# Performance work log

Measured on AMD Instinct MI355X. Metric: run time of the kernel, lower is better.

## Reference

```python
import jax, jax.numpy as jnp
import numpy as np

IN_DIM = 512
HID = IN_DIM // 2
N_SCENES = 64
SEG_LEN = 4096
N = N_SCENES * SEG_LEN
EPS = 1e-5


def setup_inputs() -> dict:
    key = jax.random.key(0)
    ks = jax.random.split(key, 6)
    feats = jax.random.normal(ks[0], (N, IN_DIM), dtype=jnp.float32)
    offsets = (jnp.arange(N_SCENES + 1, dtype=jnp.int32) * SEG_LEN)
    ln_g = jnp.ones((IN_DIM,), jnp.float32) + 0.02 * jax.random.normal(ks[1], (IN_DIM,), jnp.float32)
    ln_b = 0.02 * jax.random.normal(ks[2], (IN_DIM,), jnp.float32)
    w1 = jax.random.normal(ks[3], (HID, IN_DIM), jnp.float32) / np.sqrt(IN_DIM)
    b1 = jnp.zeros((HID,), jnp.float32)
    w2 = jax.random.normal(ks[4], (1, HID), jnp.float32) / np.sqrt(HID)
    b2 = jnp.zeros((1,), jnp.float32)
    return {"feats": feats, "ln_g": ln_g, "ln_b": ln_b, "w1": w1, "b1": b1, "w2": w2, "b2": b2, "offsets": offsets}


def reference(feats, ln_g, ln_b, w1, b1, w2, b2, offsets):
    n = feats.shape[0]
    # segment id per point from prefix-sum offsets
    seg = jnp.searchsorted(offsets, jnp.arange(n, dtype=offsets.dtype), side="right") - 1
    # score MLP: LayerNorm -> Linear -> GELU(exact) -> Linear -> scalar
    mu = jnp.mean(feats, axis=-1, keepdims=True)
    var = jnp.mean(jnp.square(feats - mu), axis=-1, keepdims=True)
    x = (feats - mu) * jax.lax.rsqrt(var + EPS) * ln_g + ln_b
    h = jax.nn.gelu(x @ w1.T + b1, approximate=False)  # [N, HID]
    s = (h @ w2.T + b2)[:, 0]  # [N]
    # segment softmax (stable)
    smax = jax.ops.segment_max(s, seg, num_segments=N_SCENES)
    e = jnp.exp(s - smax[seg])
    denom = jax.ops.segment_sum(e, seg, num_segments=N_SCENES)
    w = e / denom[seg]
    # weighted sum per segment -> [N_SCENES, IN_DIM]
    pooled = jax.ops.segment_sum(feats * w[:, None], seg, num_segments=N_SCENES)
    return pooled
```

## Files before the change

### kernel.cpp

```cpp
#include <hip/hip_runtime.h>

#define IN_DIM 512
#define HID_DIM 256
#define ROWS 32
#define XSS 520

typedef __bf16 bf16x8 __attribute__((ext_vector_type(8)));
typedef unsigned short ushort8 __attribute__((ext_vector_type(8)));
typedef float floatx16 __attribute__((ext_vector_type(16)));

__device__ __forceinline__ unsigned short f2bf_rne(float x) {
    unsigned int u = __float_as_uint(x);
    u += 0x7FFFu + ((u >> 16) & 1u);
    return (unsigned short)(u >> 16);
}
__device__ __forceinline__ unsigned int pack_bf2(float lo, float hi) {
    const unsigned int u0 = __float_as_uint(lo) + 0x8000u;
    const unsigned int u1 = __float_as_uint(hi) + 0x8000u;
    return __builtin_amdgcn_perm(u1, u0, 0x07060302u);
}
__device__ __forceinline__ float gelu(float x) {
    const float ax = fabsf(x) * 0.70710678118654752f;
    const float t = __builtin_amdgcn_rcpf(1.0f + 0.3275911f * ax);
    const float y = t * (0.254829592f +
                    t * (-0.284496736f +
                    t * (1.421413741f +
                    t * (-1.453152027f + t * 1.061405429f))));
    const float e = __expf(-ax * ax);
    float er = 1.0f - y * e;
    er = __builtin_copysignf(er, x);
    return 0.5f * x * (1.0f + er);
}

__global__ void prep_w1_kernel(const float* __restrict__ w1, const float* __restrict__ ln_g,
                               const float* __restrict__ ln_b, const float* __restrict__ b1,
                               unsigned short* __restrict__ w1g, float* __restrict__ gw,
                               float* __restrict__ c1) {
    const int wid = threadIdx.x >> 6;
    const int lane = threadIdx.x & 63;
    const int h = blockIdx.x * 4 + wid;
    const int c8 = lane * 8;
    const float4 wv0 = *(const float4*)(w1 + (size_t)h * IN_DIM + c8);
    const float4 wv1 = *(const float4*)(w1 + (size_t)h * IN_DIM + c8 + 4);
    const float4 g0 = *(const float4*)(ln_g + c8);
    const float4 g1 = *(const float4*)(ln_g + c8 + 4);
    const float4 bb0 = *(const float4*)(ln_b + c8);
    const float4 bb1 = *(const float4*)(ln_b + c8 + 4);
    float wg[8] = {wv0.x * g0.x, wv0.y * g0.y, wv0.z * g0.z, wv0.w * g0.w,
                   wv1.x * g1.x, wv1.y * g1.y, wv1.z * g1.z, wv1.w * g1.w};
    float sg = wg[0] + wg[1] + wg[2] + wg[3] + wg[4] + wg[5] + wg[6] + wg[7];
    float sb = wv0.x * bb0.x + wv0.y * bb0.y + wv0.z * bb0.z + wv0.w * bb0.w +
               wv1.x * bb1.x + wv1.y * bb1.y + wv1.z * bb1.z + wv1.w * bb1.w;
    ushort8 outv;
#pragma unroll
    for (int j = 0; j < 8; j++) outv[j] = f2bf_rne(wg[j]);
    *(ushort8*)(w1g + (size_t)h * IN_DIM + c8) = outv;
    for (int m = 32; m; m >>= 1) {
        sg += __shfl_xor(sg, m);
        sb += __shfl_xor(sb, m);
    }
    if (lane == 0) {
        gw[h] = sg;
        c1[h] = sb + b1[h];
    }
}

__global__ __launch_bounds__(512, 2) void score_kernel(
    const float* __restrict__ feats, const unsigned short* __restrict__ w1g,
    const float* __restrict__ gw, const float* __restrict__ c1,
    const float* __restrict__ w2, const float* __restrict__ b2,
    float* __restrict__ s_out, int N, int ntiles) {
    __shared__ unsigned short xs[ROWS][XSS];
    __shared__ float2 stats_s[ROWS];
    __shared__ float spart[8][ROWS];

    const int tid = threadIdx.x;
    const int wid = tid >> 6;
    const int lane = tid & 63;
    const int l31 = lane & 31;
    const int hi = lane >> 5;
    const int hid = wid * 32 + l31;

    const float gwv = gw[hid];
    const float c1v = c1[hid];
    const float w2v = w2[hid];
    const float b2v = b2[0];

    bf16x8 barr[32];
    {
        const unsigned short* bp = w1g + (size_t)hid * IN_DIM + hi * 8;
#pragma unroll
        for (int ki = 0; ki < 32; ki++)
            barr[ki] = __builtin_bit_cast(bf16x8, *(const ushort8*)(bp + ki * 16));
    }

    const int srow = tid >> 4;
    const int schunk = tid & 15;

    for (int t = blockIdx.x; t < ntiles; t += gridDim.x) {
        const int row0 = t * ROWS;

        {
            size_t rg = (size_t)(row0 + srow);
            if (rg >= (size_t)N) rg = (size_t)N - 1;
            const float* fp = feats + rg * IN_DIM + schunk * 4;
            float4 f[8];
#pragma unroll
            for (int j = 0; j < 8; j++) f[j] = *(const float4*)(fp + j * 64);
            float sf = 0.0f, qf = 0.0f;
#pragma unroll
            for (int j = 0; j < 8; j++) {
                sf += f[j].x + f[j].y + f[j].z + f[j].w;
                qf = fmaf(f[j].x, f[j].x, qf);
                qf = fmaf(f[j].y, f[j].y, qf);
                qf = fmaf(f[j].z, f[j].z, qf);
                qf = fmaf(f[j].w, f[j].w, qf);
            }
#pragma unroll
            for (int j = 0; j < 8; j++) {
                uint2 p;
                p.x = pack_bf2(f[j].x, f[j].y);
                p.y = pack_bf2(f[j].z, f[j].w);
                *(uint2*)&xs[srow][j * 64 + schunk * 4] = p;
            }
#pragma unroll
            for (int m = 1; m < 16; m <<= 1) {
                sf += __shfl_xor(sf, m);
                qf += __shfl_xor(qf, m);
            }
            if (schunk == 0) {
                const float mu = sf * (1.0f / IN_DIM);
                const float var = fmaxf(qf * (1.0f / IN_DIM) - mu * mu, 0.0f);
                stats_s[srow] = make_float2(mu, rsqrtf(var + 1e-5f));
            }
        }
        __syncthreads();

        floatx16 acc = (floatx16)(0.0f);
        {
            const unsigned short* ap = &xs[l31][hi * 8];
#pragma unroll
            for (int ki = 0; ki < 32; ki++) {
                const bf16x8 af = __builtin_bit_cast(bf16x8, *(const ushort8*)(ap + ki * 16));
                acc = __builtin_amdgcn_mfma_f32_32x32x16_bf16(af, barr[ki], acc, 0, 0, 0);
            }
        }

        float tv[16];
#pragma unroll
        for (int r = 0; r < 16; r++) {
            const int row = (r & 3) + 8 * (r >> 2) + 4 * hi;
            const float2 st = stats_s[row];
            const float hv = st.y * (acc[r] - st.x * gwv) + c1v;
            tv[r] = gelu(hv) * w2v;
        }
#pragma unroll
        for (int m = 1; m < 32; m <<= 1)
#pragma unroll
            for (int r = 0; r < 16; r++) tv[r] += __shfl_xor(tv[r], m);
        if (l31 == 0) {
#pragma unroll
            for (int r = 0; r < 16; r++)
                spart[wid][(r & 3) + 8 * (r >> 2) + 4 * hi] = tv[r];
        }
        __syncthreads();
        if (tid < ROWS) {
            const int row = row0 + tid;
            if (row < N) {
                float sv = b2v;
#pragma unroll
                for (int w = 0; w < 8; w++) sv += spart[w][tid];
                s_out[row] = sv;
            }
        }
    }
}

__global__ void segstat_kernel(const float* __restrict__ s, const int* __restrict__ offsets,
                               float* __restrict__ smax, float* __restrict__ denom, int nseg) {
    const int seg = blockIdx.x;
    const int st = offsets[seg];
    const int en = offsets[seg + 1];
    const int tid = threadIdx.x;
    __shared__ float red[8];
    float m = -3.4e38f;
    for (int i = st + tid; i < en; i += 256) m = fmaxf(m, s[i]);
    for (int mm = 32; mm; mm >>= 1) m = fmaxf(m, __shfl_xor(m, mm));
    if ((tid & 63) == 0) red[tid >> 6] = m;
    __syncthreads();
    const float M = fmaxf(fmaxf(red[0], red[1]), fmaxf(red[2], red[3]));
    float sum = 0.0f;
    for (int i = st + tid; i < en; i += 256) sum += expf(s[i] - M);
    for (int mm = 32; mm; mm >>= 1) sum += __shfl_xor(sum, mm);
    if ((tid & 63) == 0) red[4 + (tid >> 6)] = sum;
    __syncthreads();
    if (tid == 0) {
        smax[seg] = M;
        denom[seg] = red[4] + red[5] + red[6] + red[7];
    }
}

#define CHUNK 256
__global__ __launch_bounds__(256) void pool_kernel(
    const float* __restrict__ feats, const float* __restrict__ s,
    const float* __restrict__ smax, const float* __restrict__ denom,
    const int* __restrict__ offsets, int nseg, float* __restrict__ out, int N) {
    __shared__ float wbuf[CHUNK];
    __shared__ int sbuf[CHUNK];
    const int tid = threadIdx.x;
    const int r0 = blockIdx.x * CHUNK;
    const int nrows = min(CHUNK, N - r0);

    {
        const int row = r0 + tid;
        float wv = 0.0f;
        int sg = 0;
        if (row < N) {
            int lo = 0, hiq = nseg;
            while (hiq - lo > 1) {
                const int mid = (lo + hiq) >> 1;
                if (offsets[mid] <= row) lo = mid; else hiq = mid;
            }
            sg = lo;
            wv = expf(s[row] - smax[sg]) / denom[sg];
        }
        wbuf[tid] = wv;
        sbuf[tid] = sg;
    }
    __syncthreads();

    const int c4 = (tid & 127) * 4;
    const int half = tid >> 7;
    const int rs = half * (CHUNK / 2);
    const int re = min(rs + CHUNK / 2, nrows);
    if (re <= rs) return;

    if (sbuf[0] == sbuf[nrows - 1]) {
        const int seg = sbuf[0];
        float ax = 0.0f, ay = 0.0f, az = 0.0f, aw = 0.0f;
        const float* fp = feats + (size_t)r0 * IN_DIM + c4;
#pragma unroll 4
        for (int r = rs; r < re; r++) {
            const float4 f = *(const float4*)(fp + (size_t)r * IN_DIM);
            const float wv = wbuf[r];
            ax = fmaf(wv, f.x, ax);
            ay = fmaf(wv, f.y, ay);
            az = fmaf(wv, f.z, az);
            aw = fmaf(wv, f.w, aw);
        }
        float* op = out + (size_t)seg * IN_DIM + c4;
        atomicAdd(op + 0, ax);
        atomicAdd(op + 1, ay);
        atomicAdd(op + 2, az);
        atomicAdd(op + 3, aw);
    } else {
        for (int r = rs; r < re; r++) {
            const float4 f = *(const float4*)(feats + (size_t)(r0 + r) * IN_DIM + c4);
            const float wv = wbuf[r];
            float* op = out + (size_t)sbuf[r] * IN_DIM + c4;
            atomicAdd(op + 0, wv * f.x);
            atomicAdd(op + 1, wv * f.y);
            atomicAdd(op + 2, wv * f.z);
            atomicAdd(op + 3, wv * f.w);
        }
    }
}

extern "C" void kernel_launch(void* const* d_in, const int* in_sizes, int n_in,
                              void* d_out, int out_size, void* d_ws, size_t ws_size,
                              hipStream_t stream) {
    const float* feats = (const float*)d_in[0];
    const float* ln_g = (const float*)d_in[1];
    const float* ln_b = (const float*)d_in[2];
    const float* w1 = (const float*)d_in[3];
    const float* b1 = (const float*)d_in[4];
    const float* w2 = (const float*)d_in[5];
    const float* b2 = (const float*)d_in[6];
    const int* offsets = (const int*)d_in[7];
    const int N = in_sizes[0] / IN_DIM;
    const int nseg = in_sizes[7] - 1;
    float* out = (float*)d_out;

    char* ws = (char*)d_ws;
    unsigned short* w1g = (unsigned short*)ws;
    float* gw = (float*)(ws + (size_t)HID_DIM * IN_DIM * 2);
    float* c1 = gw + HID_DIM;
    float* s_arr = c1 + HID_DIM;
    float* smax = s_arr + N;
    float* denom = smax + nseg;

    const int ntiles = (N + ROWS - 1) / ROWS;
    int sgrid = ntiles < 2048 ? ntiles : 2048;

    hipMemsetAsync(d_out, 0, (size_t)out_size * sizeof(float), stream);
    prep_w1_kernel<<<HID_DIM / 4, 256, 0, stream>>>(w1, ln_g, ln_b, b1, w1g, gw, c1);
    score_kernel<<<sgrid, 512, 0, stream>>>(feats, w1g, gw, c1, w2, b2, s_arr, N, ntiles);
    segstat_kernel<<<nseg, 256, 0, stream>>>(s_arr, offsets, smax, denom, nseg);
    pool_kernel<<<(N + CHUNK - 1) / CHUNK, 256, 0, stream>>>(feats, s_arr, smax, denom, offsets, nseg, out, N);
}
```

Measured before the change: 901.9 us.

## Fuse scoring, online segment softmax and pooling into one split-segment kernel

Replaces the score, segstat and pool kernels with a single fused kernel. Each block owns a slice of one segment, computes the scores, keeps a running max and denominator (online softmax), and pools the bf16 copy of feats already staged in LDS. A small combine kernel then merges the per-slice partials. This removes the second full read of feats and the intermediate score array, and drops the atomics and the memset. In exchange, pooling now uses bf16-rounded feats, so precision drops. W1 is streamed from global/L2 on every tile instead of held in registers, and the grid is fixed at 1024 blocks of 256 threads, which may limit occupancy and MFMA throughput.

```diff
diff --git a/kernel.cpp b/kernel.cpp
--- a/kernel.cpp
+++ b/kernel.cpp
@@ -4,6 +4,8 @@
 #define HID_DIM 256
 #define ROWS 32
 #define XSS 520
+#define PSEG 16
+#define PSTRIDE 516
 
 typedef __bf16 bf16x8 __attribute__((ext_vector_type(8)));
 typedef unsigned short ushort8 __attribute__((ext_vector_type(8)));
@@ -65,43 +67,52 @@
     }
 }
 
-__global__ __launch_bounds__(512, 2) void score_kernel(
+__global__ __launch_bounds__(256, 4) void fused_kernel(
     const float* __restrict__ feats, const unsigned short* __restrict__ w1g,
     const float* __restrict__ gw, const float* __restrict__ c1,
     const float* __restrict__ w2, const float* __restrict__ b2,
-    float* __restrict__ s_out, int N, int ntiles) {
+    const int* __restrict__ offsets, float* __restrict__ partials, int N) {
     __shared__ unsigned short xs[ROWS][XSS];
+    __shared__ float spart[4][ROWS];
     __shared__ float2 stats_s[ROWS];
-    __shared__ float spart[8][ROWS];
+    __shared__ float wbuf[ROWS];
+    __shared__ float sMx, sDn, sAl;
 
     const int tid = threadIdx.x;
     const int wid = tid >> 6;
     const int lane = tid & 63;
     const int l31 = lane & 31;
     const int hi = lane >> 5;
-    const int hid = wid * 32 + l31;
-
-    const float gwv = gw[hid];
-    const float c1v = c1[hid];
-    const float w2v = w2[hid];
+    const int seg = blockIdx.x / PSEG;
+    const int part = blockIdx.x % PSEG;
+    const int st = offsets[seg];
+    const int en = offsets[seg + 1];
+    const int len = en - st;
+    const int chunk = (len + PSEG - 1) / PSEG;
+    const int rs = st + part * chunk;
+    const int re = min(rs + chunk, en);
+    const int nt = (re > rs) ? ((re - rs + ROWS - 1) / ROWS) : 0;
+
+    const int hid0 = (wid * 2 + 0) * 32 + l31;
+    const int hid1 = (wid * 2 + 1) * 32 + l31;
+    const float gw0 = gw[hid0], gw1 = gw[hid1];
+    const float c10 = c1[hid0], c11 = c1[hid1];
+    const float w20 = w2[hid0], w21 = w2[hid1];
     const float b2v = b2[0];
 
-    bf16x8 barr[32];
-    {
-        const unsigned short* bp = w1g + (size_t)hid * IN_DIM + hi * 8;
-#pragma unroll
-        for (int ki = 0; ki < 32; ki++)
-            barr[ki] = __builtin_bit_cast(bf16x8, *(const ushort8*)(bp + ki * 16));
-    }
-
-    const int srow = tid >> 4;
+    float O0 = 0.0f, O1 = 0.0f;
+    if (tid == 0) { sMx = -3.0e38f; sDn = 0.0f; }
+
+    const int srow4 = tid >> 4;
     const int schunk = tid & 15;
 
-    for (int t = blockIdx.x; t < ntiles; t += gridDim.x) {
-        const int row0 = t * ROWS;
-
-        {
-            size_t rg = (size_t)(row0 + srow);
+    for (int t = 0; t < nt; t++) {
+        const int row0 = rs + t * ROWS;
+
+#pragma unroll
+        for (int p = 0; p < 2; p++) {
+            const int r = p * 16 + srow4;
+            size_t rg = (size_t)(row0 + r);
             if (rg >= (size_t)N) rg = (size_t)N - 1;
             const float* fp = feats + rg * IN_DIM + schunk * 4;
             float4 f[8];
@@ -118,10 +129,10 @@
             }
 #pragma unroll
             for (int j = 0; j < 8; j++) {
-                uint2 p;
-                p.x = pack_bf2(f[j].x, f[j].y);
-                p.y = pack_bf2(f[j].z, f[j].w);
-                *(uint2*)&xs[srow][j * 64 + schunk * 4] = p;
+                uint2 pk;
+                pk.x = pack_bf2(f[j].x, f[j].y);
+                pk.y = pack_bf2(f[j].z, f[j].w);
+                *(uint2*)&xs[r][j * 64 + schunk * 4] = pk;
             }
 #pragma unroll
             for (int m = 1; m < 16; m <<= 1) {
@@ -131,18 +142,31 @@
             if (schunk == 0) {
                 const float mu = sf * (1.0f / IN_DIM);
                 const float var = fmaxf(qf * (1.0f / IN_DIM) - mu * mu, 0.0f);
-                stats_s[srow] = make_float2(mu, rsqrtf(var + 1e-5f));
-            }
-        }
-        __syncthreads();
-
-        floatx16 acc = (floatx16)(0.0f);
+                stats_s[r] = make_float2(mu, rsqrtf(var + 1e-5f));
+            }
+        }
+        __syncthreads();
+
+        floatx16 acc0 = (floatx16)(0.0f);
+        floatx16 acc1 = (floatx16)(0.0f);
         {
+            const unsigned short* bp0 = w1g + (size_t)hid0 * IN_DIM + hi * 8;
+            const unsigned short* bp1 = w1g + (size_t)hid1 * IN_DIM + hi * 8;
             const unsigned short* ap = &xs[l31][hi * 8];
-#pragma unroll
+            bf16x8 b0 = __builtin_bit_cast(bf16x8, *(const ushort8*)bp0);
+            bf16x8 b1 = __builtin_bit_cast(bf16x8, *(const ushort8*)bp1);
+#pragma unroll 4
             for (int ki = 0; ki < 32; ki++) {
-                const bf16x8 af = __builtin_bit_cast(bf16x8, *(const ushort8*)(ap + ki * 16));
-                acc = __builtin_amdgcn_mfma_f32_32x32x16_bf16(af, barr[ki], acc, 0, 0, 0);
+                const bf16x8 a = __builtin_bit_cast(bf16x8, *(const ushort8*)(ap + ki * 16));
+                bf16x8 n0 = b0, n1 = b1;
+                if (ki < 31) {
+                    n0 = __builtin_bit_cast(bf16x8, *(const ushort8*)(bp0 + (ki + 1) * 16));
+                    n1 = __builtin_bit_cast(bf16x8, *(const ushort8*)(bp1 + (ki + 1) * 16));
+                }
+                acc0 = __builtin_amdgcn_mfma_f32_32x32x16_bf16(a, b0, acc0, 0, 0, 0);
+                acc1 = __builtin_amdgcn_mfma_f32_32x32x16_bf16(a, b1, acc1, 0, 0, 0);
+                b0 = n0;
+                b1 = n1;
             }
         }
 
@@ -150,9 +174,10 @@
 #pragma unroll
         for (int r = 0; r < 16; r++) {
             const int row = (r & 3) + 8 * (r >> 2) + 4 * hi;
-            const float2 st = stats_s[row];
-            const float hv = st.y * (acc[r] - st.x * gwv) + c1v;
-            tv[r] = gelu(hv) * w2v;
+            const float2 stt = stats_s[row];
+            const float h0 = stt.y * (acc0[r] - stt.x * gw0) + c10;
+            const float h1 = stt.y * (acc1[r] - stt.x * gw1) + c11;
+            tv[r] = gelu(h0) * w20 + gelu(h1) * w21;
         }
 #pragma unroll
         for (int m = 1; m < 32; m <<= 1)
@@ -164,106 +189,70 @@
                 spart[wid][(r & 3) + 8 * (r >> 2) + 4 * hi] = tv[r];
         }
         __syncthreads();
-        if (tid < ROWS) {
-            const int row = row0 + tid;
-            if (row < N) {
-                float sv = b2v;
-#pragma unroll
-                for (int w = 0; w < 8; w++) sv += spart[w][tid];
-                s_out[row] = sv;
-            }
-        }
-    }
-}
-
-__global__ void segstat_kernel(const float* __restrict__ s, const int* __restrict__ offsets,
-                               float* __restrict__ smax, float* __restrict__ denom, int nseg) {
+
+        if (tid < 32) {
+            float sv = spart[0][tid] + spart[1][tid] + spart[2][tid] + spart[3][tid] + b2v;
+            if (row0 + tid >= re) sv = -3.0e38f;
+            float mt = sv;
+#pragma unroll
+            for (int m = 1; m < 32; m <<= 1) mt = fmaxf(mt, __shfl_xor(mt, m));
+            const float Mold = sMx;
+            const float Mnew = fmaxf(Mold, mt);
+            const float al = __expf(Mold - Mnew);
+            const float w = __expf(sv - Mnew);
+            wbuf[tid] = w;
+            float wsum = w;
+#pragma unroll
+            for (int m = 1; m < 32; m <<= 1) wsum += __shfl_xor(wsum, m);
+            if (tid == 0) {
+                sDn = sDn * al + wsum;
+                sMx = Mnew;
+                sAl = al;
+            }
+        }
+        __syncthreads();
+
+        {
+            const float al = sAl;
+            O0 *= al;
+            O1 *= al;
+#pragma unroll 8
+            for (int r = 0; r < ROWS; r++) {
+                const unsigned int d = *(const unsigned int*)&xs[r][tid * 2];
+                const float w = wbuf[r];
+                O0 = fmaf(w, __uint_as_float(d << 16), O0);
+                O1 = fmaf(w, __uint_as_float(d & 0xffff0000u), O1);
+            }
+        }
+        __syncthreads();
+    }
+
+    float* pp = partials + (size_t)blockIdx.x * PSTRIDE;
+    pp[2 * tid] = O0;
+    pp[2 * tid + 1] = O1;
+    if (tid == 0) {
+        pp[512] = sMx;
+        pp[513] = sDn;
+    }
+}
+
+__global__ void combine_kernel(const float* __restrict__ partials, float* __restrict__ out) {
     const int seg = blockIdx.x;
-    const int st = offsets[seg];
-    const int en = offsets[seg + 1];
-    const int tid = threadIdx.x;
-    __shared__ float red[8];
-    float m = -3.4e38f;
-    for (int i = st + tid; i < en; i += 256) m = fmaxf(m, s[i]);
-    for (int mm = 32; mm; mm >>= 1) m = fmaxf(m, __shfl_xor(m, mm));
-    if ((tid & 63) == 0) red[tid >> 6] = m;
-    __syncthreads();
-    const float M = fmaxf(fmaxf(red[0], red[1]), fmaxf(red[2], red[3]));
-    float sum = 0.0f;
-    for (int i = st + tid; i < en; i += 256) sum += expf(s[i] - M);
-    for (int mm = 32; mm; mm >>= 1) sum += __shfl_xor(sum, mm);
-    if ((tid & 63) == 0) red[4 + (tid >> 6)] = sum;
-    __syncthreads();
-    if (tid == 0) {
-        smax[seg] = M;
-        denom[seg] = red[4] + red[5] + red[6] + red[7];
-    }
-}
-
-#define CHUNK 256
-__global__ __launch_bounds__(256) void pool_kernel(
-    const float* __restrict__ feats, const float* __restrict__ s,
-    const float* __restrict__ smax, const float* __restrict__ denom,
-    const int* __restrict__ offsets, int nseg, float* __restrict__ out, int N) {
-    __shared__ float wbuf[CHUNK];
-    __shared__ int sbuf[CHUNK];
-    const int tid = threadIdx.x;
-    const int r0 = blockIdx.x * CHUNK;
-    const int nrows = min(CHUNK, N - r0);
-
-    {
-        const int row = r0 + tid;
-        float wv = 0.0f;
-        int sg = 0;
-        if (row < N) {
-            int lo = 0, hiq = nseg;
-            while (hiq - lo > 1) {
-                const int mid = (lo + hiq) >> 1;
-                if (offsets[mid] <= row) lo = mid; else hiq = mid;
-            }
-            sg = lo;
-            wv = expf(s[row] - smax[sg]) / denom[sg];
-        }
-        wbuf[tid] = wv;
-        sbuf[tid] = sg;
-    }
-    __syncthreads();
-
-    const int c4 = (tid & 127) * 4;
-    const int half = tid >> 7;
-    const int rs = half * (CHUNK / 2);
-    const int re = min(rs + CHUNK / 2, nrows);
-    if (re <= rs) return;
-
-    if (sbuf[0] == sbuf[nrows - 1]) {
-        const int seg = sbuf[0];
-        float ax = 0.0f, ay = 0.0f, az = 0.0f, aw = 0.0f;
-        const float* fp = feats + (size_t)r0 * IN_DIM + c4;
-#pragma unroll 4
-        for (int r = rs; r < re; r++) {
-            const float4 f = *(const float4*)(fp + (size_t)r * IN_DIM);
-            const float wv = wbuf[r];
-            ax = fmaf(wv, f.x, ax);
-            ay = fmaf(wv, f.y, ay);
-            az = fmaf(wv, f.z, az);
-            aw = fmaf(wv, f.w, aw);
-        }
-        float* op = out + (size_t)seg * IN_DIM + c4;
-        atomicAdd(op + 0, ax);
-        atomicAdd(op + 1, ay);
-        atomicAdd(op + 2, az);
-        atomicAdd(op + 3, aw);
-    } else {
-        for (int r = rs; r < re; r++) {
-            const float4 f = *(const float4*)(feats + (size_t)(r0 + r) * IN_DIM + c4);
-            const float wv = wbuf[r];
-            float* op = out + (size_t)sbuf[r] * IN_DIM + c4;
-            atomicAdd(op + 0, wv * f.x);
-            atomicAdd(op + 1, wv * f.y);
-            atomicAdd(op + 2, wv * f.z);
-            atomicAdd(op + 3, wv * f.w);
-        }
-    }
+    const int t = threadIdx.x;
+    const float* base = partials + (size_t)seg * PSEG * PSTRIDE;
+    float M = -3.0e38f;
+#pragma unroll
+    for (int p = 0; p < PSEG; p++) M = fmaxf(M, base[p * PSTRIDE + 512]);
+    float D = 0.0f, a0 = 0.0f, a1 = 0.0f;
+#pragma unroll
+    for (int p = 0; p < PSEG; p++) {
+        const float e = __expf(base[p * PSTRIDE + 512] - M);
+        D += e * base[p * PSTRIDE + 513];
+        a0 += e * base[p * PSTRIDE + 2 * t];
+        a1 += e * base[p * PSTRIDE + 2 * t + 1];
+    }
+    out[(size_t)seg * IN_DIM + 2 * t] = a0 / D;
+    out[(size_t)seg * IN_DIM + 2 * t + 1] = a1 / D;
 }
 
 extern "C" void kernel_launch(void* const* d_in, const int* in_sizes, int n_in,
@@ -285,16 +274,10 @@
     unsigned short* w1g = (unsigned short*)ws;
     float* gw = (float*)(ws + (size_t)HID_DIM * IN_DIM * 2);
     float* c1 = gw + HID_DIM;
-    float* s_arr = c1 + HID_DIM;
-    float* smax = s_arr + N;
-    float* denom = smax + nseg;
-
-    const int ntiles = (N + ROWS - 1) / ROWS;
-    int sgrid = ntiles < 2048 ? ntiles : 2048;
-
-    hipMemsetAsync(d_out, 0, (size_t)out_size * sizeof(float), stream);
+    float* partials = c1 + HID_DIM;
+
     prep_w1_kernel<<<HID_DIM / 4, 256, 0, stream>>>(w1, ln_g, ln_b, b1, w1g, gw, c1);
-    score_kernel<<<sgrid, 512, 0, stream>>>(feats, w1g, gw, c1, w2, b2, s_arr, N, ntiles);
-    segstat_kernel<<<nseg, 256, 0, stream>>>(s_arr, offsets, smax, denom, nseg);
-    pool_kernel<<<(N + CHUNK - 1) / CHUNK, 256, 0, stream>>>(feats, s_arr, smax, denom, offsets, nseg, out, N);
-}
+    fused_kernel<<<nseg * PSEG, 256, 0, stream>>>(feats, w1g, gw, c1, w2, b2, offsets,
+                                                  partials, N);
+    combine_kernel<<<nseg, 256, 0, stream>>>(partials, out);
+}
```

New measurement: 884.3 us. No clear change (-1.9%).
